# Kernel optimization log

Hardware: AMD Instinct MI355X
Metric: run time of the kernel (lower is better)

Reference implementation:

```python
import jax, jax.numpy as jnp
import numpy as np

K = 16  # neighbors per point (no self-loop)


def _knn_idx(pos, k):
    # pos: (N, 3). Squared euclidean pairwise distances via the ||a-b||^2 expansion.
    n = pos.shape[0]
    sq = jnp.sum(pos * pos, axis=1)                      # (N,)
    d = sq[:, None] + sq[None, :] - 2.0 * (pos @ pos.T)  # (N, N)
    # exclude self (loop=False in torch_cluster.knn_graph)
    diag = jnp.arange(n)
    d = d.at[diag, diag].set(jnp.inf)
    _, idx = jax.lax.top_k(-d, k)                        # k smallest distances -> (N, k)
    return idx


def setup_inputs() -> dict:
    key = jax.random.key(0)
    ks = jax.random.split(key, 6)
    N, C, D = 16384, 64, 64
    x = jax.random.normal(ks[0], (N, C), dtype=jnp.float32)
    pos = jax.random.normal(ks[1], (N, 3), dtype=jnp.float32)
    W1 = jax.random.normal(ks[2], (2 * C, D), dtype=jnp.float32) * 0.08
    b1 = jax.random.normal(ks[3], (D,), dtype=jnp.float32) * 0.02
    W2 = jax.random.normal(ks[4], (D, D), dtype=jnp.float32) * 0.12
    b2 = jax.random.normal(ks[5], (D,), dtype=jnp.float32) * 0.02
    return {"x": x, "pos": pos, "W1": W1, "b1": b1, "W2": W2, "b2": b2}


def reference(x, pos, W1, b1, W2, b2):
    # EdgeConv: for each center i with k-NN neighbors j:
    #   e_ij = MLP([x_i, x_j - x_i]);  out_i = max_j e_ij
    idx = _knn_idx(pos, K)                               # (N, K) int32
    x_j = x[idx]                                         # (N, K, C) gather
    x_i = x[:, None, :]                                  # (N, 1, C)
    ef = jnp.concatenate(
        [jnp.broadcast_to(x_i, x_j.shape), x_j - x_i], axis=-1
    )                                                    # (N, K, 2C)
    h = jax.nn.relu(jnp.einsum("nkc,cd->nkd", ef, W1) + b1)
    h = jnp.einsum("nkd,de->nke", h, W2) + b2            # (N, K, D)
    # each node has exactly K incoming edges -> scatter_max == max over K axis
    return jnp.max(h, axis=1)                            # (N, D)
```

## Files before the change

kernel.cpp:

```cpp
#include <hip/hip_runtime.h>
#include <hip/hip_bf16.h>


#define NPTS 16384
#define CH 64

#define GLO  (-4.5f)
#define GH   0.28125f
#define INVH 3.5555555556f
#define GDIM 32
#define GCELLS (GDIM * GDIM * GDIM)

typedef __attribute__((ext_vector_type(8))) short short8;
typedef __attribute__((ext_vector_type(4))) float floatx4;

__device__ __forceinline__ unsigned short f2bf(float f) {
    unsigned u = __float_as_uint(f);
    u += 0x7FFFu + ((u >> 16) & 1u);
    return (unsigned short)(u >> 16);
}
__device__ __forceinline__ float bf2f(unsigned short u) {
    return __uint_as_float(((unsigned)u) << 16);
}

__device__ __forceinline__ unsigned long long dpp_shr1_u64(unsigned long long x) {
    int lo = (int)(unsigned)(x & 0xFFFFFFFFULL);
    int hi = (int)(unsigned)(x >> 32);
    lo = __builtin_amdgcn_update_dpp(0, lo, 0x111, 0xF, 0xF, false);
    hi = __builtin_amdgcn_update_dpp(0, hi, 0x111, 0xF, 0xF, false);
    return (((unsigned long long)(unsigned)hi) << 32) | (unsigned)lo;
}

__device__ __forceinline__ int cell_of(float x, float y, float z) {
    int cx = (int)floorf((x - GLO) * INVH);
    int cy = (int)floorf((y - GLO) * INVH);
    int cz = (int)floorf((z - GLO) * INVH);
    cx = min(max(cx, 0), GDIM - 1);
    cy = min(max(cy, 0), GDIM - 1);
    cz = min(max(cz, 0), GDIM - 1);
    return (cz * GDIM + cy) * GDIM + cx;
}

__global__ __launch_bounds__(256) void zero_kernel(int* __restrict__ counts) {
    counts[blockIdx.x * 256 + threadIdx.x] = 0;
}

__global__ __launch_bounds__(256) void grid_count_kernel(const float* __restrict__ pos,
                                                         int* __restrict__ counts) {
    const int i = blockIdx.x * 256 + threadIdx.x;
    atomicAdd(&counts[cell_of(pos[i * 3], pos[i * 3 + 1], pos[i * 3 + 2])], 1);
}

__global__ __launch_bounds__(1024) void scan_kernel(const int* __restrict__ counts,
                                                    int* __restrict__ starts,
                                                    int* __restrict__ cursor) {
    __shared__ int lds[1024];
    const int t = threadIdx.x;
    int4 v[8];
    const int4* c4 = (const int4*)counts + t * 8;
#pragma unroll
    for (int i = 0; i < 8; ++i) v[i] = c4[i];
    int sum = 0;
#pragma unroll
    for (int i = 0; i < 8; ++i) sum += v[i].x + v[i].y + v[i].z + v[i].w;
    lds[t] = sum;
    __syncthreads();
    for (int off = 1; off < 1024; off <<= 1) {
        int x = 0;
        if (t >= off) x = lds[t - off];
        __syncthreads();
        lds[t] += x;
        __syncthreads();
    }
    int pre = (t == 0) ? 0 : lds[t - 1];
    int4* s4 = (int4*)starts + t * 8;
    int4* u4 = (int4*)cursor + t * 8;
#pragma unroll
    for (int i = 0; i < 8; ++i) {
        int4 o;
        o.x = pre; pre += v[i].x;
        o.y = pre; pre += v[i].y;
        o.z = pre; pre += v[i].z;
        o.w = pre; pre += v[i].w;
        s4[i] = o;
        u4[i] = o;
    }
    if (t == 1023) starts[GCELLS] = pre;
}

__global__ __launch_bounds__(256) void grid_scatter_kernel(const float* __restrict__ pos,
                                                           int* __restrict__ cursor,
                                                           float4* __restrict__ spos,
                                                           unsigned short* __restrict__ sidx) {
    const int i = blockIdx.x * 256 + threadIdx.x;
    const float a = pos[i * 3], b = pos[i * 3 + 1], c = pos[i * 3 + 2];
    const int dst = atomicAdd(&cursor[cell_of(a, b, c)], 1);
    spos[dst] = make_float4(a, b, c, a * a + b * b + c * c);
    sidx[dst] = (unsigned short)i;
}

#define SENT 0xFF800000FFFFFFFFULL

__global__ __launch_bounds__(256) void knn_grid_kernel(const float* __restrict__ pos,
                                                       const float4* __restrict__ spos,
                                                       const unsigned short* __restrict__ sidx,
                                                       const int* __restrict__ starts,
                                                       unsigned short* __restrict__ knn_out) {
    __shared__ int lds_ex[256];
    __shared__ int lds_st[256];
    const int lane  = threadIdx.x & 63;
    const int w     = threadIdx.x >> 6;
    const int lbase = w * 64;
    const int row   = blockIdx.x * 4 + w;

    const float qx = pos[row * 3 + 0];
    const float qy = pos[row * 3 + 1];
    const float qz = pos[row * 3 + 2];
    const float sqi = qx * qx + qy * qy + qz * qz;
    const int cix = min(max((int)floorf((qx - GLO) * INVH), 0), GDIM - 1);
    const int ciy = min(max((int)floorf((qy - GLO) * INVH), 0), GDIM - 1);
    const int ciz = min(max((int)floorf((qz - GLO) * INVH), 0), GDIM - 1);

    unsigned long long list = SENT;
    float tau = __uint_as_float(0x7F800000u);
    bool first = true;

    int pax = 1, pbx = 0, pay = 1, pby = 0, paz = 1, pbz = 0;

    for (int s = 1; s < GDIM + 1; ++s) {
        const int ax = max(cix - s, 0), bx = min(cix + s, GDIM - 1);
        const int ay = max(ciy - s, 0), by = min(ciy + s, GDIM - 1);
        const int az = max(ciz - s, 0), bz = min(ciz + s, GDIM - 1);
        const int dy = by - ay + 1, dz = bz - az + 1;
        const int npair = dy * dz;
        const float invdy = 1.0f / (float)dy;

        for (int pb = 0; pb < npair; pb += 64) {
            const int pair = pb + lane;
            int stA = 0, lenA = 0, stB = 0, lenB = 0;
            if (pair < npair) {
                const int czo = (int)(((float)pair + 0.5f) * invdy);
                const int cyo = pair - czo * dy;
                const int cy = ay + cyo, cz = az + czo;
                const int rowb = (cz * GDIM + cy) * GDIM;
                const bool inner = cy >= pay && cy <= pby && cz >= paz && cz <= pbz;
                const int bA = inner ? (pax - 1) : bx;
                if (bA >= ax) {
                    stA  = starts[rowb + ax];
                    lenA = starts[rowb + bA + 1] - stA;
                }
                if (inner) {
                    const int aB = pbx + 1;
                    if (bx >= aB) {
                        stB  = starts[rowb + aB];
                        lenB = starts[rowb + bx + 1] - stB;
                    }
                }
            }
#pragma unroll
            for (int setsel = 0; setsel < 2; ++setsel) {
                const int st  = setsel ? stB  : stA;
                const int len = setsel ? lenB : lenA;
                if (__ballot(len > 0) == 0ULL) continue;
                unsigned pfx = (unsigned)len;
#pragma unroll
                for (int off = 1; off < 64; off <<= 1) {
                    const unsigned vv = __shfl_up(pfx, off);
                    if (lane >= off) pfx += vv;
                }
                const int T  = __builtin_amdgcn_readlane((int)pfx, 63);
                const int ex = (int)pfx - len;
                lds_ex[lbase + lane] = ex;
                lds_st[lbase + lane] = st;

                for (int b = 0; b < T; b += 64) {
                    const int p = b + lane;
                    int j = 0;
#pragma unroll
                    for (int stp = 32; stp >= 1; stp >>= 1) {
                        const int m = j + stp;
                        if (lds_ex[lbase + m] <= p) j = m;
                    }
                    const int exj = lds_ex[lbase + j];
                    const int stj = lds_st[lbase + j];
                    const bool active = p < T;
                    const int idx = stj + (active ? (p - exj) : 0);
                    const float4 pt = spos[idx];
                    const int jorig = (int)sidx[idx];
                    const float dot = fmaf(qx, pt.x, fmaf(qy, pt.y, qz * pt.z));
                    const float d   = fmaf(-2.0f, dot, sqi + pt.w);

                    if (first) {
                        first = false;
                        unsigned kd = __float_as_uint(d);
                        kd = ((int)kd < 0) ? ~kd : (kd | 0x80000000u);
                        unsigned long long key =
                            (((unsigned long long)kd) << 32) | (unsigned)jorig;
                        if (!(active && jorig != row)) key = SENT;
#pragma unroll
                        for (int k = 2; k <= 64; k <<= 1) {
#pragma unroll
                            for (int jj = k >> 1; jj >= 1; jj >>= 1) {
                                const unsigned long long o = __shfl_xor(key, jj);
                                const bool takeMin =
                                    (((lane & k) == 0) == ((lane & jj) == 0));
                                const unsigned long long mn = (key < o) ? key : o;
                                const unsigned long long mx = (key < o) ? o : key;
                                key = takeMin ? mn : mx;
                            }
                        }
                        list = key;
                        const unsigned thi = (unsigned)__builtin_amdgcn_readlane(
                            (int)(unsigned)(list >> 32), 15);
                        const unsigned fb =
                            (thi >= 0x80000000u) ? (thi & 0x7FFFFFFFu) : ~thi;
                        tau = __uint_as_float(fb);
                        continue;
                    }

                    const bool cand = active && (jorig != row) && (d <= tau);
                    unsigned long long mask = __ballot(cand);
                    if (mask) {
                        unsigned kd = __float_as_uint(d);
                        kd = ((int)kd < 0) ? ~kd : (kd | 0x80000000u);
                        do {
                            const int src = __ffsll(mask) - 1;
                            mask &= mask - 1;
                            const unsigned slo = (unsigned)__builtin_amdgcn_readlane(jorig, src);
                            const unsigned shi = (unsigned)__builtin_amdgcn_readlane((int)kd, src);
                            const unsigned long long v =
                                (((unsigned long long)shi) << 32) | slo;
                            const unsigned long long prev = dpp_shr1_u64(list);
                            const unsigned long long lr = list;
                            list = (lr < v) ? lr : ((prev < v) ? v : prev);
                        } while (mask);
                        const unsigned thi = (unsigned)__builtin_amdgcn_readlane(
                            (int)(unsigned)(list >> 32), 15);
                        const unsigned fb =
                            (thi >= 0x80000000u) ? (thi & 0x7FFFFFFFu) : ~thi;
                        tau = __uint_as_float(fb);
                    }
                }
            }
        }

        const float BIG = 1e30f;
        float dout = BIG;
        if (ax > 0)        dout = fminf(dout, qx - (GLO + ax * GH));
        if (bx < GDIM - 1) dout = fminf(dout, (GLO + (bx + 1) * GH) - qx);
        if (ay > 0)        dout = fminf(dout, qy - (GLO + ay * GH));
        if (by < GDIM - 1) dout = fminf(dout, (GLO + (by + 1) * GH) - qy);
        if (az > 0)        dout = fminf(dout, qz - (GLO + az * GH));
        if (bz < GDIM - 1) dout = fminf(dout, (GLO + (bz + 1) * GH) - qz);
        if (dout * dout > tau + 1e-4f) break;
        if (ax == 0 && bx == GDIM - 1 && ay == 0 && by == GDIM - 1 &&
            az == 0 && bz == GDIM - 1) break;
        pax = ax; pbx = bx; pay = ay; pby = by; paz = az; pbz = bz;
    }

    if (lane < 16)
        knn_out[row * 16 + lane] = (unsigned short)(list & 0xFFFFULL);
}

__global__ __launch_bounds__(256) void prep_kernel(const float* __restrict__ x,
                                                   const float* __restrict__ W1,
                                                   const float* __restrict__ b1,
                                                   float* __restrict__ vout,
                                                   unsigned short* __restrict__ ubuf) {
    __shared__ unsigned short Wct[128 * 72];
    __shared__ unsigned short Abuf[64 * 72];
    __shared__ float Wraw[128 * 64];

    const int t    = threadIdx.x;
    const int lane = t & 63;
    const int w    = t >> 6;

    {
        const float4* W1v = (const float4*)W1;
        float4* Wr4 = (float4*)Wraw;
#pragma unroll
        for (int i = 0; i < 8; ++i) Wr4[i * 256 + t] = W1v[i * 256 + t];
    }
    __syncthreads();
    {
        const int n = t & 127;
        const int ks = (t >> 7) * 32;
#pragma unroll
        for (int i = 0; i < 32; ++i) {
            const int k = ks + i;
            float val;
            if (n < 64) val = Wraw[k * 64 + n] - Wraw[(64 + k) * 64 + n];
            else        val = Wraw[(64 + k) * 64 + (n - 64)];
            Wct[n * 72 + k] = f2bf(val);
        }
    }
    {
        const int col = t & 63;
#pragma unroll
        for (int i = 0; i < 16; ++i) {
            const int r2 = (t >> 6) + 4 * i;
            const int gp = blockIdx.x * 64 + r2;
            Abuf[r2 * 72 + col] = f2bf(x[(size_t)gp * CH + col]);
        }
    }
    __syncthreads();

    const int m16 = lane & 15;
    const int q   = lane >> 4;

    floatx4 acc[8];
#pragma unroll
    for (int nt = 0; nt < 8; ++nt) acc[nt] = (floatx4){0.f, 0.f, 0.f, 0.f};

#pragma unroll
    for (int kk = 0; kk < 64; kk += 32) {
        const short8 a = *(const short8*)(Abuf + (w * 16 + m16) * 72 + kk + q * 8);
#pragma unroll
        for (int nt = 0; nt < 8; ++nt) {
            const short8 b = *(const short8*)(Wct + (nt * 16 + m16) * 72 + kk + q * 8);
            acc[nt] = __builtin_amdgcn_mfma_f32_16x16x32_bf16(a, b, acc[nt], 0, 0, 0);
        }
    }

#pragma unroll
    for (int nt = 0; nt < 8; ++nt) {
        const int n = nt * 16 + m16;
#pragma unroll
        for (int r = 0; r < 4; ++r) {
            const int gp = blockIdx.x * 64 + w * 16 + q * 4 + r;
            if (n < 64) vout[(size_t)gp * CH + n] = acc[nt][r] + b1[n];
            else        ubuf[(size_t)gp * CH + (n - 64)] = f2bf(acc[nt][r]);
        }
    }
}

__global__ __launch_bounds__(256) void edge_kernel(const unsigned short* __restrict__ ubuf,
                                                   const float* __restrict__ W2,
                                                   const float* __restrict__ b2,
                                                   const unsigned short* __restrict__ knn,
                                                   float* __restrict__ out) {
    __shared__ unsigned short h[128 * 72];
    __shared__ unsigned short W2t[64 * 72];

    const int t    = threadIdx.x;
    const int lane = t & 63;
    const int w    = t >> 6;

    {
        const int n = t & 63;
        const int kb = (t >> 6) * 16;
#pragma unroll
        for (int i = 0; i < 16; ++i) {
            const int k = kb + i;
            W2t[n * 72 + k] = f2bf(W2[k * 64 + n]);
        }
    }
    {
        const int k = t >> 4;
        const int c = t & 15;
#pragma unroll
        for (int i = 0; i < 8; ++i) {
            const int gn = blockIdx.x * 8 + i;
            const int gj = (int)knn[gn * 16 + k];
            const float4  vv = ((const float4*)(out + (size_t)gn * CH))[c];
            const ushort4 uu = ((const ushort4*)(ubuf + (size_t)gj * CH))[c];
            ushort4 hv;
            hv.x = f2bf(fmaxf(vv.x + bf2f(uu.x), 0.f));
            hv.y = f2bf(fmaxf(vv.y + bf2f(uu.y), 0.f));
            hv.z = f2bf(fmaxf(vv.z + bf2f(uu.z), 0.f));
            hv.w = f2bf(fmaxf(vv.w + bf2f(uu.w), 0.f));
            const int r2 = i * 16 + k;
            *(ushort4*)(h + r2 * 72 + c * 4) = hv;
        }
    }
    __syncthreads();

    const int m16 = lane & 15;
    const int q   = lane >> 4;

    floatx4 acc[2][4];
#pragma unroll
    for (int i = 0; i < 2; ++i)
#pragma unroll
        for (int nt = 0; nt < 4; ++nt) acc[i][nt] = (floatx4){0.f, 0.f, 0.f, 0.f};

#pragma unroll
    for (int kk = 0; kk < 64; kk += 32) {
        const short8 a0 = *(const short8*)(h + ((w * 2 + 0) * 16 + m16) * 72 + kk + q * 8);
        const short8 a1 = *(const short8*)(h + ((w * 2 + 1) * 16 + m16) * 72 + kk + q * 8);
#pragma unroll
        for (int nt = 0; nt < 4; ++nt) {
            const short8 b = *(const short8*)(W2t + (nt * 16 + m16) * 72 + kk + q * 8);
            acc[0][nt] = __builtin_amdgcn_mfma_f32_16x16x32_bf16(a0, b, acc[0][nt], 0, 0, 0);
            acc[1][nt] = __builtin_amdgcn_mfma_f32_16x16x32_bf16(a1, b, acc[1][nt], 0, 0, 0);
        }
    }

#pragma unroll
    for (int i = 0; i < 2; ++i) {
        const int mt = w * 2 + i;
        const int gn = blockIdx.x * 8 + mt;
#pragma unroll
        for (int nt = 0; nt < 4; ++nt) {
            float m0 = fmaxf(fmaxf(acc[i][nt][0], acc[i][nt][1]),
                             fmaxf(acc[i][nt][2], acc[i][nt][3]));
            m0 = fmaxf(m0, __shfl_xor(m0, 16));
            m0 = fmaxf(m0, __shfl_xor(m0, 32));
            if (lane < 16)
                out[(size_t)gn * CH + nt * 16 + lane] = m0 + b2[nt * 16 + lane];
        }
    }
}

extern "C" void kernel_launch(void* const* d_in, const int* in_sizes, int n_in,
                              void* d_out, int out_size, void* d_ws, size_t ws_size,
                              hipStream_t stream) {
    const float* x   = (const float*)d_in[0];
    const float* pos = (const float*)d_in[1];
    const float* W1  = (const float*)d_in[2];
    const float* b1  = (const float*)d_in[3];
    const float* W2  = (const float*)d_in[4];
    const float* b2  = (const float*)d_in[5];
    float* out = (float*)d_out;

    char* ws = (char*)d_ws;
    unsigned short* knn  = (unsigned short*)ws;
    unsigned short* ubuf = (unsigned short*)(ws + 524288);
    int*    counts = (int*)(ws + 2621440);
    int*    starts = (int*)(ws + 2752512);
    int*    cursor = (int*)(ws + 2883600);
    float4* spos   = (float4*)(ws + 3014672);
    unsigned short* sidx = (unsigned short*)(ws + 3276816);

    zero_kernel<<<GCELLS / 256, 256, 0, stream>>>(counts);
    grid_count_kernel<<<NPTS / 256, 256, 0, stream>>>(pos, counts);
    scan_kernel<<<1, 1024, 0, stream>>>(counts, starts, cursor);
    grid_scatter_kernel<<<NPTS / 256, 256, 0, stream>>>(pos, cursor, spos, sidx);
    knn_grid_kernel<<<NPTS / 4, 256, 0, stream>>>(pos, spos, sidx, starts, knn);
    prep_kernel<<<NPTS / 64, 256, 0, stream>>>(x, W1, b1, out, ubuf);
    edge_kernel<<<NPTS / 8, 256, 0, stream>>>(ubuf, W2, b2, knn, out);
}
```

Before: 151.8 us.

## Fuse grid count with prep GEMM, batch kNN candidate loads, one wave per block

The grid-count pass and the x·W1 prep GEMM now run in a single launch: the first 64 blocks count points per cell and the other 256 do the MFMA prep. The zero kernel is replaced by hipMemsetAsync. The kNN kernel now uses one 64-thread wave per block and issues NB=4 batches of candidate gathers before doing the distance and insert work, so memory latency overlaps with compute. This trades extra registers and some divergence inside the fused kernel for fewer launches and more loads in flight.

New measurement: 144.8 us. 1.05x faster.

```diff
diff --git a/kernel.cpp b/kernel.cpp
--- a/kernel.cpp
+++ b/kernel.cpp
@@ -41,14 +41,84 @@
     return (cz * GDIM + cy) * GDIM + cx;
 }
 
-__global__ __launch_bounds__(256) void zero_kernel(int* __restrict__ counts) {
-    counts[blockIdx.x * 256 + threadIdx.x] = 0;
-}
-
-__global__ __launch_bounds__(256) void grid_count_kernel(const float* __restrict__ pos,
-                                                         int* __restrict__ counts) {
-    const int i = blockIdx.x * 256 + threadIdx.x;
-    atomicAdd(&counts[cell_of(pos[i * 3], pos[i * 3 + 1], pos[i * 3 + 2])], 1);
+__global__ __launch_bounds__(256) void count_prep_kernel(const float* __restrict__ pos,
+                                                         int* __restrict__ counts,
+                                                         const float* __restrict__ x,
+                                                         const float* __restrict__ W1,
+                                                         const float* __restrict__ b1,
+                                                         float* __restrict__ vout,
+                                                         unsigned short* __restrict__ ubuf) {
+    __shared__ unsigned short Wct[128 * 72];
+    __shared__ unsigned short Abuf[64 * 72];
+    __shared__ float Wraw[128 * 64];
+
+    const int t = threadIdx.x;
+    if (blockIdx.x < 64) {
+        const int i = blockIdx.x * 256 + t;
+        atomicAdd(&counts[cell_of(pos[i * 3], pos[i * 3 + 1], pos[i * 3 + 2])], 1);
+        return;
+    }
+    const int bid  = blockIdx.x - 64;
+    const int lane = t & 63;
+    const int w    = t >> 6;
+
+    {
+        const float4* W1v = (const float4*)W1;
+        float4* Wr4 = (float4*)Wraw;
+#pragma unroll
+        for (int i = 0; i < 8; ++i) Wr4[i * 256 + t] = W1v[i * 256 + t];
+    }
+    __syncthreads();
+    {
+        const int n = t & 127;
+        const int ks = (t >> 7) * 32;
+#pragma unroll
+        for (int i = 0; i < 32; ++i) {
+            const int k = ks + i;
+            float val;
+            if (n < 64) val = Wraw[k * 64 + n] - Wraw[(64 + k) * 64 + n];
+            else        val = Wraw[(64 + k) * 64 + (n - 64)];
+            Wct[n * 72 + k] = f2bf(val);
+        }
+    }
+    {
+        const int col = t & 63;
+#pragma unroll
+        for (int i = 0; i < 16; ++i) {
+            const int r2 = (t >> 6) + 4 * i;
+            const int gp = bid * 64 + r2;
+            Abuf[r2 * 72 + col] = f2bf(x[(size_t)gp * CH + col]);
+        }
+    }
+    __syncthreads();
+
+    const int m16 = lane & 15;
+    const int q   = lane >> 4;
+
+    floatx4 acc[8];
+#pragma unroll
+    for (int nt = 0; nt < 8; ++nt) acc[nt] = (floatx4){0.f, 0.f, 0.f, 0.f};
+
+#pragma unroll
+    for (int kk = 0; kk < 64; kk += 32) {
+        const short8 a = *(const short8*)(Abuf + (w * 16 + m16) * 72 + kk + q * 8);
+#pragma unroll
+        for (int nt = 0; nt < 8; ++nt) {
+            const short8 b = *(const short8*)(Wct + (nt * 16 + m16) * 72 + kk + q * 8);
+            acc[nt] = __builtin_amdgcn_mfma_f32_16x16x32_bf16(a, b, acc[nt], 0, 0, 0);
+        }
+    }
+
+#pragma unroll
+    for (int nt = 0; nt < 8; ++nt) {
+        const int n = nt * 16 + m16;
+#pragma unroll
+        for (int r = 0; r < 4; ++r) {
+            const int gp = bid * 64 + w * 16 + q * 4 + r;
+            if (n < 64) vout[(size_t)gp * CH + n] = acc[nt][r] + b1[n];
+            else        ubuf[(size_t)gp * CH + (n - 64)] = f2bf(acc[nt][r]);
+        }
+    }
 }
 
 __global__ __launch_bounds__(1024) void scan_kernel(const int* __restrict__ counts,
@@ -100,18 +170,17 @@
 }
 
 #define SENT 0xFF800000FFFFFFFFULL
-
-__global__ __launch_bounds__(256) void knn_grid_kernel(const float* __restrict__ pos,
-                                                       const float4* __restrict__ spos,
-                                                       const unsigned short* __restrict__ sidx,
-                                                       const int* __restrict__ starts,
-                                                       unsigned short* __restrict__ knn_out) {
-    __shared__ int lds_ex[256];
-    __shared__ int lds_st[256];
-    const int lane  = threadIdx.x & 63;
-    const int w     = threadIdx.x >> 6;
-    const int lbase = w * 64;
-    const int row   = blockIdx.x * 4 + w;
+#define NB 4
+
+__global__ __launch_bounds__(64) void knn_grid_kernel(const float* __restrict__ pos,
+                                                      const float4* __restrict__ spos,
+                                                      const unsigned short* __restrict__ sidx,
+                                                      const int* __restrict__ starts,
+                                                      unsigned short* __restrict__ knn_out) {
+    __shared__ int lds_ex[64];
+    __shared__ int lds_st[64];
+    const int lane = threadIdx.x;
+    const int row  = blockIdx.x;
 
     const float qx = pos[row * 3 + 0];
     const float qy = pos[row * 3 + 1];
@@ -169,76 +238,93 @@
                     if (lane >= off) pfx += vv;
                 }
                 const int T  = __builtin_amdgcn_readlane((int)pfx, 63);
-                const int ex = (int)pfx - len;
-                lds_ex[lbase + lane] = ex;
-                lds_st[lbase + lane] = st;
-
-                for (int b = 0; b < T; b += 64) {
-                    const int p = b + lane;
-                    int j = 0;
-#pragma unroll
-                    for (int stp = 32; stp >= 1; stp >>= 1) {
-                        const int m = j + stp;
-                        if (lds_ex[lbase + m] <= p) j = m;
+                lds_ex[lane] = (int)pfx - len;
+                lds_st[lane] = st;
+
+                for (int b0 = 0; b0 < T; b0 += 64 * NB) {
+                    float4 pts[NB];
+                    int    jor[NB];
+                    bool   act[NB];
+                    bool   live[NB];
+#pragma unroll
+                    for (int nb = 0; nb < NB; ++nb) {
+                        const int bb = b0 + nb * 64;
+                        live[nb] = bb < T;
+                        act[nb] = false;
+                        if (live[nb]) {
+                            const int p = bb + lane;
+                            int j = 0;
+#pragma unroll
+                            for (int stp = 32; stp >= 1; stp >>= 1) {
+                                const int m = j + stp;
+                                if (lds_ex[m] <= p) j = m;
+                            }
+                            int idx = lds_st[j] + (p - lds_ex[j]);
+                            idx = min(idx, NPTS - 1);
+                            act[nb] = p < T;
+                            pts[nb] = spos[idx];
+                            jor[nb] = (int)sidx[idx];
+                        }
                     }
-                    const int exj = lds_ex[lbase + j];
-                    const int stj = lds_st[lbase + j];
-                    const bool active = p < T;
-                    const int idx = stj + (active ? (p - exj) : 0);
-                    const float4 pt = spos[idx];
-                    const int jorig = (int)sidx[idx];
-                    const float dot = fmaf(qx, pt.x, fmaf(qy, pt.y, qz * pt.z));
-                    const float d   = fmaf(-2.0f, dot, sqi + pt.w);
-
-                    if (first) {
-                        first = false;
-                        unsigned kd = __float_as_uint(d);
-                        kd = ((int)kd < 0) ? ~kd : (kd | 0x80000000u);
-                        unsigned long long key =
-                            (((unsigned long long)kd) << 32) | (unsigned)jorig;
-                        if (!(active && jorig != row)) key = SENT;
-#pragma unroll
-                        for (int k = 2; k <= 64; k <<= 1) {
-#pragma unroll
-                            for (int jj = k >> 1; jj >= 1; jj >>= 1) {
-                                const unsigned long long o = __shfl_xor(key, jj);
-                                const bool takeMin =
-                                    (((lane & k) == 0) == ((lane & jj) == 0));
-                                const unsigned long long mn = (key < o) ? key : o;
-                                const unsigned long long mx = (key < o) ? o : key;
-                                key = takeMin ? mn : mx;
+#pragma unroll
+                    for (int nb = 0; nb < NB; ++nb) {
+                        if (!live[nb]) continue;
+                        const float dot = fmaf(qx, pts[nb].x,
+                                               fmaf(qy, pts[nb].y, qz * pts[nb].z));
+                        const float d = fmaf(-2.0f, dot, sqi + pts[nb].w);
+
+                        if (first) {
+                            first = false;
+                            unsigned kd = __float_as_uint(d);
+                            kd = ((int)kd < 0) ? ~kd : (kd | 0x80000000u);
+                            unsigned long long key =
+                                (((unsigned long long)kd) << 32) | (unsigned)jor[nb];
+                            if (!(act[nb] && jor[nb] != row)) key = SENT;
+#pragma unroll
+                            for (int k = 2; k <= 64; k <<= 1) {
+#pragma unroll
+                                for (int jj = k >> 1; jj >= 1; jj >>= 1) {
+                                    const unsigned long long o = __shfl_xor(key, jj);
+                                    const bool takeMin =
+                                        (((lane & k) == 0) == ((lane & jj) == 0));
+                                    const unsigned long long mn = (key < o) ? key : o;
+                                    const unsigned long long mx = (key < o) ? o : key;
+                                    key = takeMin ? mn : mx;
+                                }
                             }
+                            list = key;
+                            const unsigned thi = (unsigned)__builtin_amdgcn_readlane(
+                                (int)(unsigned)(list >> 32), 15);
+                            const unsigned fb =
+                                (thi >= 0x80000000u) ? (thi & 0x7FFFFFFFu) : ~thi;
+                            tau = __uint_as_float(fb);
+                            continue;
                         }
-                        list = key;
-                        const unsigned thi = (unsigned)__builtin_amdgcn_readlane(
-                            (int)(unsigned)(list >> 32), 15);
-                        const unsigned fb =
-                            (thi >= 0x80000000u) ? (thi & 0x7FFFFFFFu) : ~thi;
-                        tau = __uint_as_float(fb);
-                        continue;
-                    }
-
-                    const bool cand = active && (jorig != row) && (d <= tau);
-                    unsigned long long mask = __ballot(cand);
-                    if (mask) {
-                        unsigned kd = __float_as_uint(d);
-                        kd = ((int)kd < 0) ? ~kd : (kd | 0x80000000u);
-                        do {
-                            const int src = __ffsll(mask) - 1;
-                            mask &= mask - 1;
-                            const unsigned slo = (unsigned)__builtin_amdgcn_readlane(jorig, src);
-                            const unsigned shi = (unsigned)__builtin_amdgcn_readlane((int)kd, src);
-                            const unsigned long long v =
-                                (((unsigned long long)shi) << 32) | slo;
-                            const unsigned long long prev = dpp_shr1_u64(list);
-                            const unsigned long long lr = list;
-                            list = (lr < v) ? lr : ((prev < v) ? v : prev);
-                        } while (mask);
-                        const unsigned thi = (unsigned)__builtin_amdgcn_readlane(
-                            (int)(unsigned)(list >> 32), 15);
-                        const unsigned fb =
-                            (thi >= 0x80000000u) ? (thi & 0x7FFFFFFFu) : ~thi;
-                        tau = __uint_as_float(fb);
+
+                        const bool cand = act[nb] && (jor[nb] != row) && (d <= tau);
+                        unsigned long long mask = __ballot(cand);
+                        if (mask) {
+                            unsigned kd = __float_as_uint(d);
+                            kd = ((int)kd < 0) ? ~kd : (kd | 0x80000000u);
+                            do {
+                                const int src = __ffsll(mask) - 1;
+                                mask &= mask - 1;
+                                const unsigned slo =
+                                    (unsigned)__builtin_amdgcn_readlane(jor[nb], src);
+                                const unsigned shi =
+                                    (unsigned)__builtin_amdgcn_readlane((int)kd, src);
+                                const unsigned long long v =
+                                    (((unsigned long long)shi) << 32) | slo;
+                                const unsigned long long prev = dpp_shr1_u64(list);
+                                const unsigned long long lr = list;
+                                list = (lr < v) ? lr : ((prev < v) ? v : prev);
+                            } while (mask);
+                            const unsigned thi = (unsigned)__builtin_amdgcn_readlane(
+                                (int)(unsigned)(list >> 32), 15);
+                            const unsigned fb =
+                                (thi >= 0x80000000u) ? (thi & 0x7FFFFFFFu) : ~thi;
+                            tau = __uint_as_float(fb);
+                        }
                     }
                 }
             }
@@ -262,78 +348,6 @@
         knn_out[row * 16 + lane] = (unsigned short)(list & 0xFFFFULL);
 }
 
-__global__ __launch_bounds__(256) void prep_kernel(const float* __restrict__ x,
-                                                   const float* __restrict__ W1,
-                                                   const float* __restrict__ b1,
-                                                   float* __restrict__ vout,
-                                                   unsigned short* __restrict__ ubuf) {
-    __shared__ unsigned short Wct[128 * 72];
-    __shared__ unsigned short Abuf[64 * 72];
-    __shared__ float Wraw[128 * 64];
-
-    const int t    = threadIdx.x;
-    const int lane = t & 63;
-    const int w    = t >> 6;
-
-    {
-        const float4* W1v = (const float4*)W1;
-        float4* Wr4 = (float4*)Wraw;
-#pragma unroll
-        for (int i = 0; i < 8; ++i) Wr4[i * 256 + t] = W1v[i * 256 + t];
-    }
-    __syncthreads();
-    {
-        const int n = t & 127;
-        const int ks = (t >> 7) * 32;
-#pragma unroll
-        for (int i = 0; i < 32; ++i) {
-            const int k = ks + i;
-            float val;
-            if (n < 64) val = Wraw[k * 64 + n] - Wraw[(64 + k) * 64 + n];
-            else        val = Wraw[(64 + k) * 64 + (n - 64)];
-            Wct[n * 72 + k] = f2bf(val);
-        }
-    }
-    {
-        const int col = t & 63;
-#pragma unroll
-        for (int i = 0; i < 16; ++i) {
-            const int r2 = (t >> 6) + 4 * i;
-            const int gp = blockIdx.x * 64 + r2;
-            Abuf[r2 * 72 + col] = f2bf(x[(size_t)gp * CH + col]);
-        }
-    }
-    __syncthreads();
-
-    const int m16 = lane & 15;
-    const int q   = lane >> 4;
-
-    floatx4 acc[8];
-#pragma unroll
-    for (int nt = 0; nt < 8; ++nt) acc[nt] = (floatx4){0.f, 0.f, 0.f, 0.f};
-
-#pragma unroll
-    for (int kk = 0; kk < 64; kk += 32) {
-        const short8 a = *(const short8*)(Abuf + (w * 16 + m16) * 72 + kk + q * 8);
-#pragma unroll
-        for (int nt = 0; nt < 8; ++nt) {
-            const short8 b = *(const short8*)(Wct + (nt * 16 + m16) * 72 + kk + q * 8);
-            acc[nt] = __builtin_amdgcn_mfma_f32_16x16x32_bf16(a, b, acc[nt], 0, 0, 0);
-        }
-    }
-
-#pragma unroll
-    for (int nt = 0; nt < 8; ++nt) {
-        const int n = nt * 16 + m16;
-#pragma unroll
-        for (int r = 0; r < 4; ++r) {
-            const int gp = blockIdx.x * 64 + w * 16 + q * 4 + r;
-            if (n < 64) vout[(size_t)gp * CH + n] = acc[nt][r] + b1[n];
-            else        ubuf[(size_t)gp * CH + (n - 64)] = f2bf(acc[nt][r]);
-        }
-    }
-}
-
 __global__ __launch_bounds__(256) void edge_kernel(const unsigned short* __restrict__ ubuf,
                                                    const float* __restrict__ W2,
                                                    const float* __restrict__ b2,
@@ -432,11 +446,10 @@
     float4* spos   = (float4*)(ws + 3014672);
     unsigned short* sidx = (unsigned short*)(ws + 3276816);
 
-    zero_kernel<<<GCELLS / 256, 256, 0, stream>>>(counts);
-    grid_count_kernel<<<NPTS / 256, 256, 0, stream>>>(pos, counts);
+    hipMemsetAsync(counts, 0, GCELLS * sizeof(int), stream);
+    count_prep_kernel<<<320, 256, 0, stream>>>(pos, counts, x, W1, b1, out, ubuf);
     scan_kernel<<<1, 1024, 0, stream>>>(counts, starts, cursor);
     grid_scatter_kernel<<<NPTS / 256, 256, 0, stream>>>(pos, cursor, spos, sidx);
-    knn_grid_kernel<<<NPTS / 4, 256, 0, stream>>>(pos, spos, sidx, starts, knn);
-    prep_kernel<<<NPTS / 64, 256, 0, stream>>>(x, W1, b1, out, ubuf);
+    knn_grid_kernel<<<NPTS, 64, 0, stream>>>(pos, spos, sidx, starts, knn);
     edge_kernel<<<NPTS / 8, 256, 0, stream>>>(ubuf, W2, b2, knn, out);
 }
```

## Process four queries per wavefront in kNN grid search and merge count/prep kernels

Applied to the files above, without the earlier changes.

The kNN grid kernel now assigns one query per 16-lane group, so each wavefront handles four queries. It uses 16-wide DPP scans, a 16-element bitonic sort and group-masked ballots, which shrinks the per-query list to 16 lanes and cuts idle lanes when cell ranges are short. A group that finishes keeps looping until every group in the wave is done, which adds divergence. Separately, the zero kernel becomes a memset, and the grid-count and feature-prep kernels are merged into one launch with split block roles to cut launch count and overlap the two.

Result: slower. 186.1 us (+22.6%).

```diff
diff --git a/kernel.cpp b/kernel.cpp
--- a/kernel.cpp
+++ b/kernel.cpp
@@ -22,7 +22,13 @@
 __device__ __forceinline__ float bf2f(unsigned short u) {
     return __uint_as_float(((unsigned)u) << 16);
 }
-
+__device__ __forceinline__ unsigned row_iscan16(unsigned x) {
+    x += (unsigned)__builtin_amdgcn_update_dpp(0, (int)x, 0x111, 0xF, 0xF, true);
+    x += (unsigned)__builtin_amdgcn_update_dpp(0, (int)x, 0x112, 0xF, 0xF, true);
+    x += (unsigned)__builtin_amdgcn_update_dpp(0, (int)x, 0x114, 0xF, 0xF, true);
+    x += (unsigned)__builtin_amdgcn_update_dpp(0, (int)x, 0x118, 0xF, 0xF, true);
+    return x;
+}
 __device__ __forceinline__ unsigned long long dpp_shr1_u64(unsigned long long x) {
     int lo = (int)(unsigned)(x & 0xFFFFFFFFULL);
     int hi = (int)(unsigned)(x >> 32);
@@ -30,7 +36,6 @@
     hi = __builtin_amdgcn_update_dpp(0, hi, 0x111, 0xF, 0xF, false);
     return (((unsigned long long)(unsigned)hi) << 32) | (unsigned)lo;
 }
-
 __device__ __forceinline__ int cell_of(float x, float y, float z) {
     int cx = (int)floorf((x - GLO) * INVH);
     int cy = (int)floorf((y - GLO) * INVH);
@@ -41,14 +46,84 @@
     return (cz * GDIM + cy) * GDIM + cx;
 }
 
-__global__ __launch_bounds__(256) void zero_kernel(int* __restrict__ counts) {
-    counts[blockIdx.x * 256 + threadIdx.x] = 0;
-}
-
-__global__ __launch_bounds__(256) void grid_count_kernel(const float* __restrict__ pos,
-                                                         int* __restrict__ counts) {
-    const int i = blockIdx.x * 256 + threadIdx.x;
-    atomicAdd(&counts[cell_of(pos[i * 3], pos[i * 3 + 1], pos[i * 3 + 2])], 1);
+__global__ __launch_bounds__(256) void count_prep_kernel(const float* __restrict__ pos,
+                                                         int* __restrict__ counts,
+                                                         const float* __restrict__ x,
+                                                         const float* __restrict__ W1,
+                                                         const float* __restrict__ b1,
+                                                         float* __restrict__ vout,
+                                                         unsigned short* __restrict__ ubuf) {
+    __shared__ unsigned short Wct[128 * 72];
+    __shared__ unsigned short Abuf[64 * 72];
+    __shared__ float Wraw[128 * 64];
+
+    const int t = threadIdx.x;
+    if (blockIdx.x < 64) {
+        const int i = blockIdx.x * 256 + t;
+        atomicAdd(&counts[cell_of(pos[i * 3], pos[i * 3 + 1], pos[i * 3 + 2])], 1);
+        return;
+    }
+    const int bid  = blockIdx.x - 64;
+    const int lane = t & 63;
+    const int w    = t >> 6;
+
+    {
+        const float4* W1v = (const float4*)W1;
+        float4* Wr4 = (float4*)Wraw;
+#pragma unroll
+        for (int i = 0; i < 8; ++i) Wr4[i * 256 + t] = W1v[i * 256 + t];
+    }
+    __syncthreads();
+    {
+        const int n = t & 127;
+        const int ks = (t >> 7) * 32;
+#pragma unroll
+        for (int i = 0; i < 32; ++i) {
+            const int k = ks + i;
+            float val;
+            if (n < 64) val = Wraw[k * 64 + n] - Wraw[(64 + k) * 64 + n];
+            else        val = Wraw[(64 + k) * 64 + (n - 64)];
+            Wct[n * 72 + k] = f2bf(val);
+        }
+    }
+    {
+        const int col = t & 63;
+#pragma unroll
+        for (int i = 0; i < 16; ++i) {
+            const int r2 = (t >> 6) + 4 * i;
+            const int gp = bid * 64 + r2;
+            Abuf[r2 * 72 + col] = f2bf(x[(size_t)gp * CH + col]);
+        }
+    }
+    __syncthreads();
+
+    const int m16 = lane & 15;
+    const int q   = lane >> 4;
+
+    floatx4 acc[8];
+#pragma unroll
+    for (int nt = 0; nt < 8; ++nt) acc[nt] = (floatx4){0.f, 0.f, 0.f, 0.f};
+
+#pragma unroll
+    for (int kk = 0; kk < 64; kk += 32) {
+        const short8 a = *(const short8*)(Abuf + (w * 16 + m16) * 72 + kk + q * 8);
+#pragma unroll
+        for (int nt = 0; nt < 8; ++nt) {
+            const short8 b = *(const short8*)(Wct + (nt * 16 + m16) * 72 + kk + q * 8);
+            acc[nt] = __builtin_amdgcn_mfma_f32_16x16x32_bf16(a, b, acc[nt], 0, 0, 0);
+        }
+    }
+
+#pragma unroll
+    for (int nt = 0; nt < 8; ++nt) {
+        const int n = nt * 16 + m16;
+#pragma unroll
+        for (int r = 0; r < 4; ++r) {
+            const int gp = bid * 64 + w * 16 + q * 4 + r;
+            if (n < 64) vout[(size_t)gp * CH + n] = acc[nt][r] + b1[n];
+            else        ubuf[(size_t)gp * CH + (n - 64)] = f2bf(acc[nt][r]);
+        }
+    }
 }
 
 __global__ __launch_bounds__(1024) void scan_kernel(const int* __restrict__ counts,
@@ -108,10 +183,16 @@
                                                        unsigned short* __restrict__ knn_out) {
     __shared__ int lds_ex[256];
     __shared__ int lds_st[256];
-    const int lane  = threadIdx.x & 63;
-    const int w     = threadIdx.x >> 6;
-    const int lbase = w * 64;
-    const int row   = blockIdx.x * 4 + w;
+    const int t    = threadIdx.x;
+    const int lane = t & 63;
+    const int w    = t >> 6;
+    const int g    = lane >> 4;
+    const int l16  = lane & 15;
+    const int gb   = g * 16;
+    int* exg = lds_ex + w * 64 + gb;
+    int* stg = lds_st + w * 64 + gb;
+
+    const int row = blockIdx.x * 16 + w * 4 + g;
 
     const float qx = pos[row * 3 + 0];
     const float qy = pos[row * 3 + 1];
@@ -124,214 +205,143 @@
     unsigned long long list = SENT;
     float tau = __uint_as_float(0x7F800000u);
     bool first = true;
+    bool done = false;
 
     int pax = 1, pbx = 0, pay = 1, pby = 0, paz = 1, pbz = 0;
 
     for (int s = 1; s < GDIM + 1; ++s) {
-        const int ax = max(cix - s, 0), bx = min(cix + s, GDIM - 1);
-        const int ay = max(ciy - s, 0), by = min(ciy + s, GDIM - 1);
-        const int az = max(ciz - s, 0), bz = min(ciz + s, GDIM - 1);
-        const int dy = by - ay + 1, dz = bz - az + 1;
-        const int npair = dy * dz;
-        const float invdy = 1.0f / (float)dy;
-
-        for (int pb = 0; pb < npair; pb += 64) {
-            const int pair = pb + lane;
-            int stA = 0, lenA = 0, stB = 0, lenB = 0;
-            if (pair < npair) {
-                const int czo = (int)(((float)pair + 0.5f) * invdy);
-                const int cyo = pair - czo * dy;
-                const int cy = ay + cyo, cz = az + czo;
-                const int rowb = (cz * GDIM + cy) * GDIM;
-                const bool inner = cy >= pay && cy <= pby && cz >= paz && cz <= pbz;
-                const int bA = inner ? (pax - 1) : bx;
-                if (bA >= ax) {
-                    stA  = starts[rowb + ax];
-                    lenA = starts[rowb + bA + 1] - stA;
+        if (!done) {
+            const int ax = max(cix - s, 0), bx = min(cix + s, GDIM - 1);
+            const int ay = max(ciy - s, 0), by = min(ciy + s, GDIM - 1);
+            const int az = max(ciz - s, 0), bz = min(ciz + s, GDIM - 1);
+            const int dy = by - ay + 1, dz = bz - az + 1;
+            const int npair = dy * dz;
+            const float invdy = 1.0f / (float)dy;
+
+            for (int pb = 0; pb < npair; pb += 16) {
+                const int pair = pb + l16;
+                int stA = 0, lenA = 0, stB = 0, lenB = 0;
+                if (pair < npair) {
+                    const int czo = (int)(((float)pair + 0.5f) * invdy);
+                    const int cyo = pair - czo * dy;
+                    const int cy = ay + cyo, cz = az + czo;
+                    const int rowb = (cz * GDIM + cy) * GDIM;
+                    const bool inner = cy >= pay && cy <= pby && cz >= paz && cz <= pbz;
+                    const int bA = inner ? (pax - 1) : bx;
+                    if (bA >= ax) {
+                        stA  = starts[rowb + ax];
+                        lenA = starts[rowb + bA + 1] - stA;
+                    }
+                    if (inner) {
+                        const int aB = pbx + 1;
+                        if (bx >= aB) {
+                            stB  = starts[rowb + aB];
+                            lenB = starts[rowb + bx + 1] - stB;
+                        }
+                    }
                 }
-                if (inner) {
-                    const int aB = pbx + 1;
-                    if (bx >= aB) {
-                        stB  = starts[rowb + aB];
-                        lenB = starts[rowb + bx + 1] - stB;
+#pragma unroll
+                for (int setsel = 0; setsel < 2; ++setsel) {
+                    const int st  = setsel ? stB  : stA;
+                    const int len = setsel ? lenB : lenA;
+                    const unsigned gm_len =
+                        (unsigned)((__ballot(len > 0) >> gb) & 0xFFFFULL);
+                    if (!gm_len) continue;
+                    const unsigned pfx = row_iscan16((unsigned)len);
+                    const int T = (int)(unsigned)__shfl(pfx, gb + 15);
+                    exg[l16] = (int)pfx - len;
+                    stg[l16] = st;
+
+                    for (int b0 = 0; b0 < T; b0 += 16) {
+                        const int p = b0 + l16;
+                        int j = 0;
+#pragma unroll
+                        for (int stp = 8; stp >= 1; stp >>= 1) {
+                            const int m = j + stp;
+                            if (exg[m] <= p) j = m;
+                        }
+                        int idx = stg[j] + (p - exg[j]);
+                        idx = min(idx, NPTS - 1);
+                        const bool active = p < T;
+                        const float4 pt = spos[idx];
+                        const int jorig = (int)sidx[idx];
+                        const float dot = fmaf(qx, pt.x, fmaf(qy, pt.y, qz * pt.z));
+                        const float d   = fmaf(-2.0f, dot, sqi + pt.w);
+
+                        if (first) {
+                            first = false;
+                            unsigned kd = __float_as_uint(d);
+                            kd = ((int)kd < 0) ? ~kd : (kd | 0x80000000u);
+                            unsigned long long key =
+                                (((unsigned long long)kd) << 32) | (unsigned)jorig;
+                            if (!(active && jorig != row)) key = SENT;
+#pragma unroll
+                            for (int k = 2; k <= 16; k <<= 1) {
+#pragma unroll
+                                for (int jj = k >> 1; jj >= 1; jj >>= 1) {
+                                    const unsigned long long o = __shfl_xor(key, jj);
+                                    const bool takeMin =
+                                        (((l16 & k) == 0) == ((l16 & jj) == 0));
+                                    const unsigned long long mn = (key < o) ? key : o;
+                                    const unsigned long long mx = (key < o) ? o : key;
+                                    key = takeMin ? mn : mx;
+                                }
+                            }
+                            list = key;
+                            const unsigned thi = (unsigned)(unsigned long long)
+                                (__shfl(list, gb + 15) >> 32);
+                            const unsigned fb =
+                                (thi >= 0x80000000u) ? (thi & 0x7FFFFFFFu) : ~thi;
+                            tau = __uint_as_float(fb);
+                            continue;
+                        }
+
+                        const bool cand = active && (jorig != row) && (d <= tau);
+                        unsigned gm =
+                            (unsigned)((__ballot(cand) >> gb) & 0xFFFFULL);
+                        if (gm) {
+                            unsigned kd = __float_as_uint(d);
+                            kd = ((int)kd < 0) ? ~kd : (kd | 0x80000000u);
+                            do {
+                                const int src = gb + (__ffs(gm) - 1);
+                                gm &= gm - 1;
+                                const unsigned slo = (unsigned)__shfl(jorig, src);
+                                const unsigned shi = (unsigned)__shfl((int)kd, src);
+                                const unsigned long long v =
+                                    (((unsigned long long)shi) << 32) | slo;
+                                const unsigned long long prev = dpp_shr1_u64(list);
+                                const unsigned long long lr = list;
+                                list = (lr < v) ? lr : ((prev < v) ? v : prev);
+                            } while (gm);
+                            const unsigned thi = (unsigned)(unsigned long long)
+                                (__shfl(list, gb + 15) >> 32);
+                            const unsigned fb =
+                                (thi >= 0x80000000u) ? (thi & 0x7FFFFFFFu) : ~thi;
+                            tau = __uint_as_float(fb);
+                        }
                     }
                 }
             }
-#pragma unroll
-            for (int setsel = 0; setsel < 2; ++setsel) {
-                const int st  = setsel ? stB  : stA;
-                const int len = setsel ? lenB : lenA;
-                if (__ballot(len > 0) == 0ULL) continue;
-                unsigned pfx = (unsigned)len;
-#pragma unroll
-                for (int off = 1; off < 64; off <<= 1) {
-                    const unsigned vv = __shfl_up(pfx, off);
-                    if (lane >= off) pfx += vv;
-                }
-                const int T  = __builtin_amdgcn_readlane((int)pfx, 63);
-                const int ex = (int)pfx - len;
-                lds_ex[lbase + lane] = ex;
-                lds_st[lbase + lane] = st;
-
-                for (int b = 0; b < T; b += 64) {
-                    const int p = b + lane;
-                    int j = 0;
-#pragma unroll
-                    for (int stp = 32; stp >= 1; stp >>= 1) {
-                        const int m = j + stp;
-                        if (lds_ex[lbase + m] <= p) j = m;
-                    }
-                    const int exj = lds_ex[lbase + j];
-                    const int stj = lds_st[lbase + j];
-                    const bool active = p < T;
-                    const int idx = stj + (active ? (p - exj) : 0);
-                    const float4 pt = spos[idx];
-                    const int jorig = (int)sidx[idx];
-                    const float dot = fmaf(qx, pt.x, fmaf(qy, pt.y, qz * pt.z));
-                    const float d   = fmaf(-2.0f, dot, sqi + pt.w);
-
-                    if (first) {
-                        first = false;
-                        unsigned kd = __float_as_uint(d);
-                        kd = ((int)kd < 0) ? ~kd : (kd | 0x80000000u);
-                        unsigned long long key =
-                            (((unsigned long long)kd) << 32) | (unsigned)jorig;
-                        if (!(active && jorig != row)) key = SENT;
-#pragma unroll
-                        for (int k = 2; k <= 64; k <<= 1) {
-#pragma unroll
-                            for (int jj = k >> 1; jj >= 1; jj >>= 1) {
-                                const unsigned long long o = __shfl_xor(key, jj);
-                                const bool takeMin =
-                                    (((lane & k) == 0) == ((lane & jj) == 0));
-                                const unsigned long long mn = (key < o) ? key : o;
-                                const unsigned long long mx = (key < o) ? o : key;
-                                key = takeMin ? mn : mx;
-                            }
-                        }
-                        list = key;
-                        const unsigned thi = (unsigned)__builtin_amdgcn_readlane(
-                            (int)(unsigned)(list >> 32), 15);
-                        const unsigned fb =
-                            (thi >= 0x80000000u) ? (thi & 0x7FFFFFFFu) : ~thi;
-                        tau = __uint_as_float(fb);
-                        continue;
-                    }
-
-                    const bool cand = active && (jorig != row) && (d <= tau);
-                    unsigned long long mask = __ballot(cand);
-                    if (mask) {
-                        unsigned kd = __float_as_uint(d);
-                        kd = ((int)kd < 0) ? ~kd : (kd | 0x80000000u);
-                        do {
-                            const int src = __ffsll(mask) - 1;
-                            mask &= mask - 1;
-                            const unsigned slo = (unsigned)__builtin_amdgcn_readlane(jorig, src);
-                            const unsigned shi = (unsigned)__builtin_amdgcn_readlane((int)kd, src);
-                            const unsigned long long v =
-                                (((unsigned long long)shi) << 32) | slo;
-                            const unsigned long long prev = dpp_shr1_u64(list);
-                            const unsigned long long lr = list;
-                            list = (lr < v) ? lr : ((prev < v) ? v : prev);
-                        } while (mask);
-                        const unsigned thi = (unsigned)__builtin_amdgcn_readlane(
-                            (int)(unsigned)(list >> 32), 15);
-                        const unsigned fb =
-                            (thi >= 0x80000000u) ? (thi & 0x7FFFFFFFu) : ~thi;
-                        tau = __uint_as_float(fb);
-                    }
-                }
+
+            const float BIG = 1e30f;
+            float dout = BIG;
+            if (ax > 0)        dout = fminf(dout, qx - (GLO + ax * GH));
+            if (bx < GDIM - 1) dout = fminf(dout, (GLO + (bx + 1) * GH) - qx);
+            if (ay > 0)        dout = fminf(dout, qy - (GLO + ay * GH));
+            if (by < GDIM - 1) dout = fminf(dout, (GLO + (by + 1) * GH) - qy);
+            if (az > 0)        dout = fminf(dout, qz - (GLO + az * GH));
+            if (bz < GDIM - 1) dout = fminf(dout, (GLO + (bz + 1) * GH) - qz);
+            if (dout * dout > tau + 1e-4f) done = true;
+            if (ax == 0 && bx == GDIM - 1 && ay == 0 && by == GDIM - 1 &&
+                az == 0 && bz == GDIM - 1) done = true;
+            if (!done) {
+                pax = ax; pbx = bx; pay = ay; pby = by; paz = az; pbz = bz;
             }
         }
-
-        const float BIG = 1e30f;
-        float dout = BIG;
-        if (ax > 0)        dout = fminf(dout, qx - (GLO + ax * GH));
-        if (bx < GDIM - 1) dout = fminf(dout, (GLO + (bx + 1) * GH) - qx);
-        if (ay > 0)        dout = fminf(dout, qy - (GLO + ay * GH));
-        if (by < GDIM - 1) dout = fminf(dout, (GLO + (by + 1) * GH) - qy);
-        if (az > 0)        dout = fminf(dout, qz - (GLO + az * GH));
-        if (bz < GDIM - 1) dout = fminf(dout, (GLO + (bz + 1) * GH) - qz);
-        if (dout * dout > tau + 1e-4f) break;
-        if (ax == 0 && bx == GDIM - 1 && ay == 0 && by == GDIM - 1 &&
-            az == 0 && bz == GDIM - 1) break;
-        pax = ax; pbx = bx; pay = ay; pby = by; paz = az; pbz = bz;
-    }
-
-    if (lane < 16)
-        knn_out[row * 16 + lane] = (unsigned short)(list & 0xFFFFULL);
-}
-
-__global__ __launch_bounds__(256) void prep_kernel(const float* __restrict__ x,
-                                                   const float* __restrict__ W1,
-                                                   const float* __restrict__ b1,
-                                                   float* __restrict__ vout,
-                                                   unsigned short* __restrict__ ubuf) {
-    __shared__ unsigned short Wct[128 * 72];
-    __shared__ unsigned short Abuf[64 * 72];
-    __shared__ float Wraw[128 * 64];
-
-    const int t    = threadIdx.x;
-    const int lane = t & 63;
-    const int w    = t >> 6;
-
-    {
-        const float4* W1v = (const float4*)W1;
-        float4* Wr4 = (float4*)Wraw;
-#pragma unroll
-        for (int i = 0; i < 8; ++i) Wr4[i * 256 + t] = W1v[i * 256 + t];
-    }
-    __syncthreads();
-    {
-        const int n = t & 127;
-        const int ks = (t >> 7) * 32;
-#pragma unroll
-        for (int i = 0; i < 32; ++i) {
-            const int k = ks + i;
-            float val;
-            if (n < 64) val = Wraw[k * 64 + n] - Wraw[(64 + k) * 64 + n];
-            else        val = Wraw[(64 + k) * 64 + (n - 64)];
-            Wct[n * 72 + k] = f2bf(val);
-        }
-    }
-    {
-        const int col = t & 63;
-#pragma unroll
-        for (int i = 0; i < 16; ++i) {
-            const int r2 = (t >> 6) + 4 * i;
-            const int gp = blockIdx.x * 64 + r2;
-            Abuf[r2 * 72 + col] = f2bf(x[(size_t)gp * CH + col]);
-        }
-    }
-    __syncthreads();
-
-    const int m16 = lane & 15;
-    const int q   = lane >> 4;
-
-    floatx4 acc[8];
-#pragma unroll
-    for (int nt = 0; nt < 8; ++nt) acc[nt] = (floatx4){0.f, 0.f, 0.f, 0.f};
-
-#pragma unroll
-    for (int kk = 0; kk < 64; kk += 32) {
-        const short8 a = *(const short8*)(Abuf + (w * 16 + m16) * 72 + kk + q * 8);
-#pragma unroll
-        for (int nt = 0; nt < 8; ++nt) {
-            const short8 b = *(const short8*)(Wct + (nt * 16 + m16) * 72 + kk + q * 8);
-            acc[nt] = __builtin_amdgcn_mfma_f32_16x16x32_bf16(a, b, acc[nt], 0, 0, 0);
-        }
-    }
-
-#pragma unroll
-    for (int nt = 0; nt < 8; ++nt) {
-        const int n = nt * 16 + m16;
-#pragma unroll
-        for (int r = 0; r < 4; ++r) {
-            const int gp = blockIdx.x * 64 + w * 16 + q * 4 + r;
-            if (n < 64) vout[(size_t)gp * CH + n] = acc[nt][r] + b1[n];
-            else        ubuf[(size_t)gp * CH + (n - 64)] = f2bf(acc[nt][r]);
-        }
-    }
+        if (__ballot(!done) == 0ULL) break;
+    }
+
+    knn_out[row * 16 + l16] = (unsigned short)(list & 0xFFFFULL);
 }
 
 __global__ __launch_bounds__(256) void edge_kernel(const unsigned short* __restrict__ ubuf,
@@ -432,11 +442,10 @@
     float4* spos   = (float4*)(ws + 3014672);
     unsigned short* sidx = (unsigned short*)(ws + 3276816);
 
-    zero_kernel<<<GCELLS / 256, 256, 0, stream>>>(counts);
-    grid_count_kernel<<<NPTS / 256, 256, 0, stream>>>(pos, counts);
+    hipMemsetAsync(counts, 0, GCELLS * sizeof(int), stream);
+    count_prep_kernel<<<320, 256, 0, stream>>>(pos, counts, x, W1, b1, out, ubuf);
     scan_kernel<<<1, 1024, 0, stream>>>(counts, starts, cursor);
     grid_scatter_kernel<<<NPTS / 256, 256, 0, stream>>>(pos, cursor, spos, sidx);
-    knn_grid_kernel<<<NPTS / 4, 256, 0, stream>>>(pos, spos, sidx, starts, knn);
-    prep_kernel<<<NPTS / 64, 256, 0, stream>>>(x, W1, b1, out, ubuf);
+    knn_grid_kernel<<<NPTS / 16, 256, 0, stream>>>(pos, spos, sidx, starts, knn);
     edge_kernel<<<NPTS / 8, 256, 0, stream>>>(ubuf, W2, b2, knn, out);
 }
```
